# Kernel optimization log

Hardware: AMD Instinct MI355X
Metric: run time of the kernel (lower is better)

The kernel has to match this reference:

```python
import jax, jax.numpy as jnp
import numpy as np

N, E = 50000, 800000
IN, HID, HEADS, OUT = 128, 64, 4, 256
HC = HID * HEADS  # 256
NEG_SLOPE = 0.2
LN_EPS = 1e-5


def setup_inputs() -> dict:
    key = jax.random.key(0)
    ks = jax.random.split(key, 20)
    s = 0.02
    inp = {
        "x": jax.random.normal(ks[0], (N, IN), jnp.float32),
        "edge_index": jax.random.randint(ks[1], (2, E), 0, N, jnp.int64),
        "w_in": jax.random.normal(ks[2], (IN, HID), jnp.float32) * s,
        "b_in": jnp.zeros((HID,), jnp.float32),
        "lin0_w": jax.random.normal(ks[3], (HID, HC), jnp.float32) * s,
        "att_src0": jax.random.normal(ks[4], (HEADS, HID), jnp.float32) * s,
        "att_dst0": jax.random.normal(ks[5], (HEADS, HID), jnp.float32) * s,
        "bias0": jnp.zeros((HC,), jnp.float32),
        "ln0_g": jnp.ones((HC,), jnp.float32),
        "ln0_b": jnp.zeros((HC,), jnp.float32),
        "lin1_w": jax.random.normal(ks[6], (HC, HC), jnp.float32) * s,
        "att_src1": jax.random.normal(ks[7], (HEADS, HID), jnp.float32) * s,
        "att_dst1": jax.random.normal(ks[8], (HEADS, HID), jnp.float32) * s,
        "bias1": jnp.zeros((HC,), jnp.float32),
        "ln1_g": jnp.ones((HC,), jnp.float32),
        "ln1_b": jnp.zeros((HC,), jnp.float32),
        "w_out": jax.random.normal(ks[9], (HC, OUT), jnp.float32) * s,
        "b_out": jnp.zeros((OUT,), jnp.float32),
    }
    return inp


def _gat_conv(x, src, dst, lin_w, att_s, att_d, bias):
    # x: [N, F_in]; src/dst: [E'] (self loops included); output [N, HEADS*HID]
    n = x.shape[0]
    h = (x @ lin_w).reshape(n, HEADS, HID)                     # [N,H,C]
    a_s = jnp.einsum('nhc,hc->nh', h, att_s)                   # [N,H]
    a_d = jnp.einsum('nhc,hc->nh', h, att_d)
    e = jax.nn.leaky_relu(a_s[src] + a_d[dst], NEG_SLOPE)      # [E',H]
    # scatter-softmax over edges grouped by destination node
    m = jax.ops.segment_max(e, dst, num_segments=n)            # [N,H]
    ex = jnp.exp(e - m[dst])
    z = jax.ops.segment_sum(ex, dst, num_segments=n)
    alpha = ex / (z[dst] + 1e-16)                              # [E',H]
    msg = h[src] * alpha[:, :, None]                           # [E',H,C]
    out = jax.ops.segment_sum(msg, dst, num_segments=n)        # [N,H,C]
    return out.reshape(n, HEADS * HID) + bias


def _layernorm(x, g, b):
    mu = x.mean(-1, keepdims=True)
    var = ((x - mu) ** 2).mean(-1, keepdims=True)
    return (x - mu) * jax.lax.rsqrt(var + LN_EPS) * g + b


def reference(x, edge_index, w_in, b_in,
              lin0_w, att_src0, att_dst0, bias0, ln0_g, ln0_b,
              lin1_w, att_src1, att_dst1, bias1, ln1_g, ln1_b,
              w_out, b_out):
    n = x.shape[0]
    # PyG GATConv adds self loops by default
    loop = jnp.arange(n, dtype=edge_index.dtype)
    src = jnp.concatenate([edge_index[0], loop])
    dst = jnp.concatenate([edge_index[1], loop])

    h = jax.nn.relu(x @ w_in + b_in)                           # input_proj + relu
    h = _gat_conv(h, src, dst, lin0_w, att_src0, att_dst0, bias0)
    h = jax.nn.relu(_layernorm(h, ln0_g, ln0_b))               # dropout: eval mode (identity)
    h = _gat_conv(h, src, dst, lin1_w, att_src1, att_dst1, bias1)
    h = jax.nn.relu(_layernorm(h, ln1_g, ln1_b))
    g = h.mean(axis=0)                                         # mean pool over nodes
    return g @ w_out + b_out                                   # [OUT]
```

## Files before the change

kernel.cpp:

```cpp
#include <hip/hip_runtime.h>

#define NN 50000
#define EE 800000
#define EP (EE + NN)
#define NH 4
#define HC 256
#define NOUT 256
#define NEG_SLOPE 0.2f
#define LN_EPS 1e-5f
#define NB 49
#define CHUNK 64
#define NPART 64

typedef unsigned short u16;
typedef __attribute__((ext_vector_type(8))) short bf16x8;
typedef __attribute__((ext_vector_type(8))) unsigned short ushort8;
typedef __attribute__((ext_vector_type(4))) float f32x4;
typedef __attribute__((ext_vector_type(2))) float f32x2;

__device__ __forceinline__ u16 f2bf(float f) {
    unsigned int u = __float_as_uint(f);
    u += 0x7fff + ((u >> 16) & 1);
    return (u16)(u >> 16);
}
__device__ __forceinline__ float bf2f(u16 s) {
    return __uint_as_float(((unsigned int)s) << 16);
}
__device__ __forceinline__ int permL(int s) {
    return (s >> 6) * 64 + (s & 3) * 16 + ((s & 63) >> 2);
}

__global__ void k_prep(const float* __restrict__ w_in, const float* __restrict__ lin0_w,
                       const float* __restrict__ lin1_w,
                       const float* __restrict__ atts0, const float* __restrict__ attd0,
                       const float* __restrict__ bias1, const float* __restrict__ ln1g,
                       const float* __restrict__ ln1b,
                       u16* __restrict__ winT, u16* __restrict__ w0T, u16* __restrict__ w1T,
                       float* __restrict__ avs, float* __restrict__ avd,
                       float* __restrict__ biasP, float* __restrict__ gP, float* __restrict__ bP,
                       int* __restrict__ deg, float* __restrict__ gaccP,
                       const int* __restrict__ raw, int* __restrict__ flag) {
    int b = blockIdx.x, t = threadIdx.x;
    if (b < 352) {
        int i = b * 256 + t;
        if (i < 8192)       { int k = i >> 6,  j = i & 63;  winT[j * 128 + k] = f2bf(w_in[i]); }
        else if (i < 24576) { int i2 = i - 8192;  int k = i2 >> 8, j = i2 & 255; w0T[j * 64 + k]  = f2bf(lin0_w[i2]); }
        else if (i < 90112) { int i2 = i - 24576; int k = i2 >> 8, j = i2 & 255; w1T[j * 256 + k] = f2bf(lin1_w[i2]); }
    } else if (b < 548) {
        int i = (b - 352) * 256 + t;
        if (i < NN) deg[i] = 0;
    } else if (b < 612) {
        gaccP[(b - 548) * 256 + t] = 0.f;
    } else if (b == 612) {
        __shared__ int any;
        if (t == 0) any = 0;
        __syncthreads();
        int found = 0;
        for (int i = t; i < 4096; i += 256)
            if (raw[2 * i + 1] != 0) found = 1;
        if (found) atomicOr(&any, 1);
        __syncthreads();
        if (t == 0) *flag = any;
    } else if (b == 613) {
        int k = t >> 2, h = t & 3;
        float ss = 0.f, dd = 0.f;
        for (int c = 0; c < 64; ++c) {
            float w = lin0_w[k * HC + h * 64 + c];
            ss += w * atts0[h * 64 + c];
            dd += w * attd0[h * 64 + c];
        }
        avs[t] = ss; avd[t] = dd;
    } else {
        int L = permL(t);
        biasP[t] = bias1[L];
        gP[t]    = ln1g[L];
        bP[t]    = ln1b[L];
    }
}

__global__ void k_hist(const int* __restrict__ raw, const int* __restrict__ flag,
                       int* __restrict__ deg) {
    int e = blockIdx.x * blockDim.x + threadIdx.x;
    if (e >= EE) return;
    int d = (*flag) ? raw[EE + e] : raw[2 * (EE + e)];
    atomicAdd(&deg[d], 1);
}

__global__ void k_scanA(const int* __restrict__ deg, int* __restrict__ tmp,
                        int* __restrict__ bsum) {
    __shared__ int ws[16];
    int lane = threadIdx.x & 63, wid = threadIdx.x >> 6;
    int i = blockIdx.x * 1024 + threadIdx.x;
    int x = (i < NN) ? deg[i] + 1 : 0;
    #pragma unroll
    for (int o = 1; o < 64; o <<= 1) {
        int t = __shfl_up(x, o, 64);
        if (lane >= o) x += t;
    }
    if (lane == 63) ws[wid] = x;
    __syncthreads();
    if (wid == 0 && lane < 16) {
        int s = ws[lane];
        #pragma unroll
        for (int o = 1; o < 16; o <<= 1) {
            int t = __shfl_up(s, o, 64);
            if (lane >= o) s += t;
        }
        ws[lane] = s;
    }
    __syncthreads();
    x += (wid > 0) ? ws[wid - 1] : 0;
    if (i < NN) tmp[i] = x;
    if (threadIdx.x == 1023) bsum[blockIdx.x] = x;
}

__global__ void k_scanC(const int* __restrict__ tmp, const int* __restrict__ bsum,
                        const int* __restrict__ deg, int* __restrict__ rowptr,
                        int* __restrict__ cursor) {
    __shared__ int soff;
    if (threadIdx.x == 0) {
        int o = 0;
        for (int j = 0; j < blockIdx.x; ++j) o += bsum[j];
        soff = o;
    }
    __syncthreads();
    int i = blockIdx.x * 1024 + threadIdx.x;
    if (i >= NN) return;
    int fin = tmp[i] + soff;
    rowptr[i + 1] = fin;
    cursor[i] = fin - (deg[i] + 1);
    if (i == 0) rowptr[0] = 0;
}

__global__ void k_scatter(const int* __restrict__ raw, const int* __restrict__ flag,
                          int* __restrict__ cursor, int* __restrict__ esrc) {
    int e = blockIdx.x * blockDim.x + threadIdx.x;
    if (e >= EP) return;
    int s, d;
    if (e >= EE) { s = e - EE; d = s; }
    else if (*flag) { s = raw[e];     d = raw[EE + e]; }
    else            { s = raw[2 * e]; d = raw[2 * (EE + e)]; }
    int pos = atomicAdd(&cursor[d], 1);
    esrc[pos] = s;
}

__global__ void k_proj_mfma(const float* __restrict__ x, const u16* __restrict__ wT,
                            const float* __restrict__ bias,
                            const float* __restrict__ avs, const float* __restrict__ avd,
                            u16* __restrict__ h0,
                            float* __restrict__ as_, float* __restrict__ ad_) {
    __shared__ float4 s_avs[64], s_avd[64];
    int wave = threadIdx.x >> 6, lane = threadIdx.x & 63;
    int lr = lane & 15, lk = lane >> 4;
    if (threadIdx.x < 64) {
        s_avs[threadIdx.x] = *(const float4*)&avs[threadIdx.x * 4];
        s_avd[threadIdx.x] = *(const float4*)&avd[threadIdx.x * 4];
    }
    __syncthreads();
    int rowbase = (blockIdx.x * 4 + wave) * 64;
    f32x4 acc[4][4];
    #pragma unroll
    for (int mf = 0; mf < 4; ++mf)
        #pragma unroll
        for (int nf = 0; nf < 4; ++nf) acc[mf][nf] = (f32x4)0.f;
    for (int kk = 0; kk < 128; kk += 32) {
        bf16x8 a[4], b[4];
        #pragma unroll
        for (int mf = 0; mf < 4; ++mf) {
            int row = rowbase + mf * 16 + lr;
            if (row < NN) {
                float4 v0 = *(const float4*)&x[(size_t)row * 128 + kk + lk * 8];
                float4 v1 = *(const float4*)&x[(size_t)row * 128 + kk + lk * 8 + 4];
                a[mf][0] = (short)f2bf(v0.x); a[mf][1] = (short)f2bf(v0.y);
                a[mf][2] = (short)f2bf(v0.z); a[mf][3] = (short)f2bf(v0.w);
                a[mf][4] = (short)f2bf(v1.x); a[mf][5] = (short)f2bf(v1.y);
                a[mf][6] = (short)f2bf(v1.z); a[mf][7] = (short)f2bf(v1.w);
            } else a[mf] = (bf16x8)(short)0;
        }
        #pragma unroll
        for (int nf = 0; nf < 4; ++nf)
            b[nf] = *(const bf16x8*)&wT[(size_t)(nf * 16 + lr) * 128 + kk + lk * 8];
        #pragma unroll
        for (int mf = 0; mf < 4; ++mf)
            #pragma unroll
            for (int nf = 0; nf < 4; ++nf)
                acc[mf][nf] = __builtin_amdgcn_mfma_f32_16x16x32_bf16(a[mf], b[nf], acc[mf][nf], 0, 0, 0);
    }
    #pragma unroll
    for (int mf = 0; mf < 4; ++mf)
        #pragma unroll
        for (int r = 0; r < 4; ++r) {
            int row = rowbase + mf * 16 + lk * 4 + r;
            float4 ps = make_float4(0.f, 0.f, 0.f, 0.f);
            float4 pd = make_float4(0.f, 0.f, 0.f, 0.f);
            #pragma unroll
            for (int nf = 0; nf < 4; ++nf) {
                int col = nf * 16 + lr;
                float v = fmaxf(acc[mf][nf][r] + bias[col], 0.f);
                if (row < NN) h0[(size_t)row * 64 + col] = f2bf(v);
                float4 vs = s_avs[col], vd = s_avd[col];
                ps.x += v * vs.x; ps.y += v * vs.y; ps.z += v * vs.z; ps.w += v * vs.w;
                pd.x += v * vd.x; pd.y += v * vd.y; pd.z += v * vd.z; pd.w += v * vd.w;
            }
            #pragma unroll
            for (int o = 1; o < 16; o <<= 1) {
                ps.x += __shfl_xor(ps.x, o, 64); ps.y += __shfl_xor(ps.y, o, 64);
                ps.z += __shfl_xor(ps.z, o, 64); ps.w += __shfl_xor(ps.w, o, 64);
                pd.x += __shfl_xor(pd.x, o, 64); pd.y += __shfl_xor(pd.y, o, 64);
                pd.z += __shfl_xor(pd.z, o, 64); pd.w += __shfl_xor(pd.w, o, 64);
            }
            if (lr == 0 && row < NN) {
                *(float4*)&as_[row * NH] = ps;
                *(float4*)&ad_[row * NH] = pd;
            }
        }
}

__global__ void k_agg64(const int* __restrict__ rowptr, const int* __restrict__ esrc,
                        const u16* __restrict__ h0, const float* __restrict__ as_,
                        const float* __restrict__ ad_, u16* __restrict__ agg) {
    __shared__ float sw[4][CHUNK][4];
    __shared__ int   ss[4][CHUNK];
    int wave = threadIdx.x >> 6, lane = threadIdx.x & 63;
    int n = blockIdx.x * 4 + wave;
    int start = rowptr[n], end = rowptr[n + 1];
    float4 adv = *(const float4*)&ad_[n * NH];
    int p = lane & 15, grp = lane >> 4;
    f32x2 acc2[4][2];
    #pragma unroll
    for (int h = 0; h < 4; ++h) {
        acc2[h][0] = (f32x2)0.f;
        acc2[h][1] = (f32x2)0.f;
    }
    float z0 = 0.f, z1 = 0.f, z2 = 0.f, z3 = 0.f;

    for (int base = start; base < end; base += CHUNK) {
        int m = end - base; if (m > CHUNK) m = CHUNK;
        {
            int s = 0; float4 w4 = make_float4(0.f, 0.f, 0.f, 0.f);
            if (lane < m) {
                s = esrc[base + lane];
                float4 asv = *(const float4*)&as_[s * NH];
                float e0 = asv.x + adv.x; e0 = e0 > 0.f ? e0 : e0 * NEG_SLOPE; w4.x = __expf(e0);
                float e1 = asv.y + adv.y; e1 = e1 > 0.f ? e1 : e1 * NEG_SLOPE; w4.y = __expf(e1);
                float e2 = asv.z + adv.z; e2 = e2 > 0.f ? e2 : e2 * NEG_SLOPE; w4.z = __expf(e2);
                float e3 = asv.w + adv.w; e3 = e3 > 0.f ? e3 : e3 * NEG_SLOPE; w4.w = __expf(e3);
            }
            ss[wave][lane] = s;
            *(float4*)&sw[wave][lane][0] = w4;
            z0 += w4.x; z1 += w4.y; z2 += w4.z; z3 += w4.w;
        }
        int e = grp;
        int s = ss[wave][e];
        float4 w4 = *(const float4*)&sw[wave][e][0];
        uint2 hv = *(const uint2*)&h0[(size_t)s * 64 + p * 4];
        int nIter = (m + 3) >> 2;
        for (int it = 0; it < nIter; ++it) {
            int en = (e + 4) & (CHUNK - 1);
            int sn = ss[wave][en];
            float4 w4n = *(const float4*)&sw[wave][en][0];
            uint2 hvn = *(const uint2*)&h0[(size_t)sn * 64 + p * 4];
            f32x2 p01, p23;
            p01[0] = __uint_as_float(hv.x << 16);
            p01[1] = __uint_as_float(hv.x & 0xffff0000u);
            p23[0] = __uint_as_float(hv.y << 16);
            p23[1] = __uint_as_float(hv.y & 0xffff0000u);
            acc2[0][0] += (f32x2)w4.x * p01; acc2[0][1] += (f32x2)w4.x * p23;
            acc2[1][0] += (f32x2)w4.y * p01; acc2[1][1] += (f32x2)w4.y * p23;
            acc2[2][0] += (f32x2)w4.z * p01; acc2[2][1] += (f32x2)w4.z * p23;
            acc2[3][0] += (f32x2)w4.w * p01; acc2[3][1] += (f32x2)w4.w * p23;
            e = en; w4 = w4n; hv = hvn;
        }
    }
    #pragma unroll
    for (int h = 0; h < 4; ++h)
        #pragma unroll
        for (int j = 0; j < 2; ++j) {
            acc2[h][j][0] += __shfl_xor(acc2[h][j][0], 16, 64);
            acc2[h][j][0] += __shfl_xor(acc2[h][j][0], 32, 64);
            acc2[h][j][1] += __shfl_xor(acc2[h][j][1], 16, 64);
            acc2[h][j][1] += __shfl_xor(acc2[h][j][1], 32, 64);
        }
    #pragma unroll
    for (int o = 32; o >= 1; o >>= 1) {
        z0 += __shfl_xor(z0, o, 64);
        z1 += __shfl_xor(z1, o, 64);
        z2 += __shfl_xor(z2, o, 64);
        z3 += __shfl_xor(z3, o, 64);
    }
    if (grp == 0) {
        float iz[4] = {1.f / (z0 + 1e-16f), 1.f / (z1 + 1e-16f),
                       1.f / (z2 + 1e-16f), 1.f / (z3 + 1e-16f)};
        #pragma unroll
        for (int h = 0; h < 4; ++h) {
            ushort4 yv;
            yv.x = f2bf(acc2[h][0][0] * iz[h]);
            yv.y = f2bf(acc2[h][0][1] * iz[h]);
            yv.z = f2bf(acc2[h][1][0] * iz[h]);
            yv.w = f2bf(acc2[h][1][1] * iz[h]);
            *(ushort4*)&agg[(size_t)n * HC + h * 64 + p * 4] = yv;
        }
    }
}

__global__ __launch_bounds__(256) void k_mid(
        const u16* __restrict__ agg, const u16* __restrict__ w0T,
        const float* __restrict__ bias0, const float* __restrict__ g0, const float* __restrict__ b0,
        const u16* __restrict__ w1T,
        const float* __restrict__ atts1, const float* __restrict__ attd1,
        unsigned int* __restrict__ hp8,
        float* __restrict__ as_, float* __restrict__ ad_) {
    __shared__ __align__(16) u16 h1sh[64 * 256];
    __shared__ float stat[64][4][2];
    __shared__ float murs[64][2];
    int wave = threadIdx.x >> 6, lane = threadIdx.x & 63;
    int lr = lane & 15, lk = lane >> 4;
    int rowbase = blockIdx.x * 64;

    f32x4 acc[4][4];
    #pragma unroll
    for (int mf = 0; mf < 4; ++mf)
        #pragma unroll
        for (int nf = 0; nf < 4; ++nf) acc[mf][nf] = (f32x4)0.f;
    for (int kk = 0; kk < 64; kk += 32) {
        bf16x8 a[4], bv[4];
        #pragma unroll
        for (int mf = 0; mf < 4; ++mf) {
            int row = rowbase + mf * 16 + lr;
            a[mf] = (row < NN) ? *(const bf16x8*)&agg[(size_t)row * HC + wave * 64 + kk + lk * 8]
                               : (bf16x8)(short)0;
        }
        #pragma unroll
        for (int nf = 0; nf < 4; ++nf)
            bv[nf] = *(const bf16x8*)&w0T[(size_t)(wave * 64 + nf * 16 + lr) * 64 + kk + lk * 8];
        #pragma unroll
        for (int mf = 0; mf < 4; ++mf)
            #pragma unroll
            for (int nf = 0; nf < 4; ++nf)
                acc[mf][nf] = __builtin_amdgcn_mfma_f32_16x16x32_bf16(a[mf], bv[nf], acc[mf][nf], 0, 0, 0);
    }
    float bcol[4];
    #pragma unroll
    for (int nf = 0; nf < 4; ++nf) bcol[nf] = bias0[wave * 64 + nf * 16 + lr];
    #pragma unroll
    for (int mf = 0; mf < 4; ++mf)
        #pragma unroll
        for (int r = 0; r < 4; ++r) {
            float s = 0.f, q = 0.f;
            #pragma unroll
            for (int nf = 0; nf < 4; ++nf) {
                float xv = acc[mf][nf][r] + bcol[nf];
                s += xv; q += xv * xv;
            }
            #pragma unroll
            for (int o = 1; o < 16; o <<= 1) {
                s += __shfl_xor(s, o, 64);
                q += __shfl_xor(q, o, 64);
            }
            if (lr == 0) {
                int row = mf * 16 + lk * 4 + r;
                stat[row][wave][0] = s;
                stat[row][wave][1] = q;
            }
        }
    __syncthreads();
    if (threadIdx.x < 64) {
        int row = threadIdx.x;
        float S = stat[row][0][0] + stat[row][1][0] + stat[row][2][0] + stat[row][3][0];
        float Q = stat[row][0][1] + stat[row][1][1] + stat[row][2][1] + stat[row][3][1];
        float mu = S * (1.f / HC);
        float var = Q * (1.f / HC) - mu * mu;
        murs[row][0] = mu;
        murs[row][1] = rsqrtf(var + LN_EPS);
    }
    __syncthreads();
    #pragma unroll
    for (int mf = 0; mf < 4; ++mf)
        #pragma unroll
        for (int r = 0; r < 4; ++r) {
            int lrow = mf * 16 + lk * 4 + r;
            float mu = murs[lrow][0], rs = murs[lrow][1];
            #pragma unroll
            for (int nf = 0; nf < 4; ++nf) {
                int col = wave * 64 + nf * 16 + lr;
                float xv = acc[mf][nf][r] + bcol[nf];
                u16 y = f2bf(fmaxf((xv - mu) * rs * g0[col] + b0[col], 0.f));
                int byte = (lrow * 512 + col * 2) ^ ((lrow & 7) << 4);
                *(u16*)((char*)h1sh + byte) = y;
            }
        }
    __syncthreads();

    f32x4 acc2[4][4];
    #pragma unroll
    for (int mf = 0; mf < 4; ++mf)
        #pragma unroll
        for (int nf = 0; nf < 4; ++nf) acc2[mf][nf] = (f32x4)0.f;
    for (int kk = 0; kk < 256; kk += 32) {
        bf16x8 a[4], bv[4];
        #pragma unroll
        for (int mf = 0; mf < 4; ++mf) {
            int row = mf * 16 + lr;
            int byte = (row * 512 + (kk + lk * 8) * 2) ^ ((row & 7) << 4);
            a[mf] = *(const bf16x8*)((const char*)h1sh + byte);
        }
        #pragma unroll
        for (int nf = 0; nf < 4; ++nf)
            bv[nf] = *(const bf16x8*)&w1T[(size_t)(wave * 64 + nf * 16 + lr) * 256 + kk + lk * 8];
        #pragma unroll
        for (int mf = 0; mf < 4; ++mf)
            #pragma unroll
            for (int nf = 0; nf < 4; ++nf)
                acc2[mf][nf] = __builtin_amdgcn_mfma_f32_16x16x32_bf16(a[mf], bv[nf], acc2[mf][nf], 0, 0, 0);
    }
    float asv[4], adv[4];
    #pragma unroll
    for (int nf = 0; nf < 4; ++nf) {
        int col = wave * 64 + nf * 16 + lr;
        asv[nf] = atts1[col];
        adv[nf] = attd1[col];
    }
    #pragma unroll
    for (int mf = 0; mf < 4; ++mf)
        #pragma unroll
        for (int r = 0; r < 4; ++r) {
            int row = rowbase + mf * 16 + lk * 4 + r;
            float v0 = acc2[mf][0][r], v1 = acc2[mf][1][r];
            float v2 = acc2[mf][2][r], v3 = acc2[mf][3][r];
            float ps = v0 * asv[0] + v1 * asv[1] + v2 * asv[2] + v3 * asv[3];
            float pd = v0 * adv[0] + v1 * adv[1] + v2 * adv[2] + v3 * adv[3];
            unsigned int pk = (unsigned int)__builtin_amdgcn_cvt_pk_fp8_f32(v0, v1, 0, false);
            pk = (unsigned int)__builtin_amdgcn_cvt_pk_fp8_f32(v2, v3, (int)pk, true);
            if (row < NN) hp8[(size_t)row * 64 + wave * 16 + lr] = pk;
            #pragma unroll
            for (int o = 1; o < 16; o <<= 1) {
                ps += __shfl_xor(ps, o, 64);
                pd += __shfl_xor(pd, o, 64);
            }
            if (lr == 0 && row < NN) {
                as_[row * NH + wave] = ps;
                ad_[row * NH + wave] = pd;
            }
        }
}

__global__ void k_agg_ln8(const int* __restrict__ rowptr, const int* __restrict__ esrc,
                          const unsigned int* __restrict__ hp8, const float* __restrict__ as_,
                          const float* __restrict__ ad_,
                          const float* __restrict__ biasP, const float* __restrict__ gP,
                          const float* __restrict__ bP, float* __restrict__ gaccP) {
    __shared__ float sw[4][CHUNK][4];
    __shared__ int   ss[4][CHUNK];
    __shared__ float pool[4][16][17];
    int wave = threadIdx.x >> 6, lane = threadIdx.x & 63;
    int n = blockIdx.x * 4 + wave;
    int start = rowptr[n], end = rowptr[n + 1];
    float4 adv = *(const float4*)&ad_[n * NH];
    int p = lane & 15, grp = lane >> 4;
    int c = p * 16, hd = p >> 2;
    f32x2 acc2[8];
    #pragma unroll
    for (int j = 0; j < 8; ++j) acc2[j] = (f32x2)0.f;
    float z0 = 0.f, z1 = 0.f, z2 = 0.f, z3 = 0.f;

    for (int base = start; base < end; base += CHUNK) {
        int m = end - base; if (m > CHUNK) m = CHUNK;
        if (lane < m) {
            int s = esrc[base + lane];
            float4 asv = *(const float4*)&as_[s * NH];
            float e0 = asv.x + adv.x; e0 = e0 > 0.f ? e0 : e0 * NEG_SLOPE; float w0 = __expf(e0);
            float e1 = asv.y + adv.y; e1 = e1 > 0.f ? e1 : e1 * NEG_SLOPE; float w1 = __expf(e1);
            float e2 = asv.z + adv.z; e2 = e2 > 0.f ? e2 : e2 * NEG_SLOPE; float w2 = __expf(e2);
            float e3 = asv.w + adv.w; e3 = e3 > 0.f ? e3 : e3 * NEG_SLOPE; float w3 = __expf(e3);
            ss[wave][lane] = s;
            *(float4*)&sw[wave][lane][0] = make_float4(w0, w1, w2, w3);
            z0 += w0; z1 += w1; z2 += w2; z3 += w3;
        }
        int e = grp;
        bool v = e < m;
        int s = v ? ss[wave][e] : 0;
        float w = v ? sw[wave][e][hd] : 0.f;
        uint4 q = *(const uint4*)&hp8[(size_t)s * 64 + p * 4];
        int nIter = (m + 3) >> 2;
        for (int it = 0; it < nIter; ++it) {
            int en = e + 4;
            bool vn = en < m;
            int sn = vn ? ss[wave][en] : 0;
            float wn = vn ? sw[wave][en][hd] : 0.f;
            uint4 qn = *(const uint4*)&hp8[(size_t)sn * 64 + p * 4];
            f32x2 wv = (f32x2)w;
            acc2[0] += wv * __builtin_amdgcn_cvt_pk_f32_fp8((int)q.x, false);
            acc2[1] += wv * __builtin_amdgcn_cvt_pk_f32_fp8((int)q.x, true);
            acc2[2] += wv * __builtin_amdgcn_cvt_pk_f32_fp8((int)q.y, false);
            acc2[3] += wv * __builtin_amdgcn_cvt_pk_f32_fp8((int)q.y, true);
            acc2[4] += wv * __builtin_amdgcn_cvt_pk_f32_fp8((int)q.z, false);
            acc2[5] += wv * __builtin_amdgcn_cvt_pk_f32_fp8((int)q.z, true);
            acc2[6] += wv * __builtin_amdgcn_cvt_pk_f32_fp8((int)q.w, false);
            acc2[7] += wv * __builtin_amdgcn_cvt_pk_f32_fp8((int)q.w, true);
            e = en; w = wn; q = qn;
        }
    }
    #pragma unroll
    for (int j = 0; j < 8; ++j) {
        acc2[j][0] += __shfl_xor(acc2[j][0], 16, 64);
        acc2[j][0] += __shfl_xor(acc2[j][0], 32, 64);
        acc2[j][1] += __shfl_xor(acc2[j][1], 16, 64);
        acc2[j][1] += __shfl_xor(acc2[j][1], 32, 64);
    }
    #pragma unroll
    for (int o = 32; o >= 1; o >>= 1) {
        z0 += __shfl_xor(z0, o, 64);
        z1 += __shfl_xor(z1, o, 64);
        z2 += __shfl_xor(z2, o, 64);
        z3 += __shfl_xor(z3, o, 64);
    }
    float zh = hd == 0 ? z0 : hd == 1 ? z1 : hd == 2 ? z2 : z3;
    float iz = 1.f / (zh + 1e-16f);
    float xv[16], sum = 0.f;
    #pragma unroll
    for (int k = 0; k < 16; ++k) { xv[k] = acc2[k >> 1][k & 1] * iz + biasP[c + k]; sum += xv[k]; }
    #pragma unroll
    for (int o = 8; o >= 1; o >>= 1) sum += __shfl_xor(sum, o, 64);
    float mu = sum * (1.f / HC);
    float vs = 0.f;
    #pragma unroll
    for (int k = 0; k < 16; ++k) { float d = xv[k] - mu; vs += d * d; }
    #pragma unroll
    for (int o = 8; o >= 1; o >>= 1) vs += __shfl_xor(vs, o, 64);
    float rs = rsqrtf(vs * (1.f / HC) + LN_EPS);
    if (grp == 0) {
        #pragma unroll
        for (int k = 0; k < 16; ++k)
            pool[wave][p][k] = fmaxf((xv[k] - mu) * rs * gP[c + k] + bP[c + k], 0.f);
    }
    __syncthreads();
    int t = threadIdx.x;
    float s = pool[0][t >> 4][t & 15] + pool[1][t >> 4][t & 15]
            + pool[2][t >> 4][t & 15] + pool[3][t >> 4][t & 15];
    atomicAdd(&gaccP[(blockIdx.x & (NPART - 1)) * 256 + t], s);
}

__global__ void k_final(const float* __restrict__ gaccP, const float* __restrict__ w,
                        const float* __restrict__ b, float* __restrict__ out) {
    __shared__ float gs[256];
    int t = threadIdx.x;
    float s = 0.f;
    for (int pp = 0; pp < NPART; ++pp) s += gaccP[pp * 256 + t];
    gs[t] = s;
    __syncthreads();
    float acc = b[t];
    for (int k = 0; k < HC; ++k)
        acc += (gs[k] * (1.f / NN)) * w[permL(k) * NOUT + t];
    out[t] = acc;
}

extern "C" void kernel_launch(void* const* d_in, const int* in_sizes, int n_in,
                              void* d_out, int out_size, void* d_ws, size_t ws_size,
                              hipStream_t stream) {
    const float* x      = (const float*)d_in[0];
    const int*   eiraw  = (const int*)d_in[1];
    const float* w_in   = (const float*)d_in[2];
    const float* b_in   = (const float*)d_in[3];
    const float* lin0_w = (const float*)d_in[4];
    const float* atts0  = (const float*)d_in[5];
    const float* attd0  = (const float*)d_in[6];
    const float* bias0  = (const float*)d_in[7];
    const float* ln0g   = (const float*)d_in[8];
    const float* ln0b   = (const float*)d_in[9];
    const float* lin1_w = (const float*)d_in[10];
    const float* atts1  = (const float*)d_in[11];
    const float* attd1  = (const float*)d_in[12];
    const float* bias1  = (const float*)d_in[13];
    const float* ln1g   = (const float*)d_in[14];
    const float* ln1b   = (const float*)d_in[15];
    const float* w_out  = (const float*)d_in[16];
    const float* b_out  = (const float*)d_in[17];
    float* out = (float*)d_out;

    char* ws = (char*)d_ws;
    size_t off = 0;
    auto alloc = [&](size_t bytes) {
        void* p = ws + off;
        off = (off + bytes + 255) & ~(size_t)255;
        return p;
    };
    int*   esrc   = (int*)  alloc((size_t)EP * 4 + 256);
    int*   deg    = (int*)  alloc((size_t)NN * 4);
    int*   cursor = (int*)  alloc((size_t)NN * 4);
    int*   tmp    = (int*)  alloc((size_t)NN * 4);
    int*   bsum   = (int*)  alloc(64 * 4);
    int*   rowptr = (int*)  alloc((size_t)(NN + 1) * 4);
    int*   flag   = (int*)  alloc(256);
    u16*   winT   = (u16*)  alloc((size_t)64 * 128 * 2);
    u16*   w0T    = (u16*)  alloc((size_t)256 * 64 * 2);
    u16*   w1T    = (u16*)  alloc((size_t)256 * 256 * 2);
    float* avs    = (float*)alloc(64 * 4 * 4);
    float* avd    = (float*)alloc(64 * 4 * 4);
    float* biasP  = (float*)alloc(HC * 4);
    float* gP     = (float*)alloc(HC * 4);
    float* bP     = (float*)alloc(HC * 4);
    u16*   h0b    = (u16*)  alloc((size_t)NN * 64 * 2);
    u16*   hpb    = (u16*)  alloc((size_t)NN * HC * 2);
    unsigned int* hp8 = (unsigned int*)alloc((size_t)NN * 64 * 4);
    float* as_    = (float*)alloc((size_t)NN * NH * 4);
    float* ad_    = (float*)alloc((size_t)NN * NH * 4);
    float* gaccP  = (float*)alloc((size_t)NPART * HC * 4);

    k_prep<<<615, 256, 0, stream>>>(w_in, lin0_w, lin1_w, atts0, attd0, bias1, ln1g, ln1b,
                                    winT, w0T, w1T, avs, avd, biasP, gP, bP,
                                    deg, gaccP, eiraw, flag);
    k_hist<<<(EE + 255) / 256, 256, 0, stream>>>(eiraw, flag, deg);
    k_scanA<<<NB, 1024, 0, stream>>>(deg, tmp, bsum);
    k_scanC<<<NB, 1024, 0, stream>>>(tmp, bsum, deg, rowptr, cursor);
    k_scatter<<<(EP + 255) / 256, 256, 0, stream>>>(eiraw, flag, cursor, esrc);

    k_proj_mfma<<<(NN + 255) / 256, 256, 0, stream>>>(x, winT, b_in, avs, avd, h0b, as_, ad_);

    k_agg64<<<NN / 4, 256, 0, stream>>>(rowptr, esrc, h0b, as_, ad_, hpb);

    k_mid<<<(NN + 63) / 64, 256, 0, stream>>>(hpb, w0T, bias0, ln0g, ln0b,
                                              w1T, atts1, attd1, hp8, as_, ad_);

    k_agg_ln8<<<NN / 4, 256, 0, stream>>>(rowptr, esrc, hp8, as_, ad_, biasP, gP, bP, gaccP);

    k_final<<<1, 256, 0, stream>>>(gaccP, w_out, b_out, out);
}
```

Measured before the change: 282.9 us.

## Fuse layer-0 edge aggregation into mid GEMM kernel via LDS tile; deepen fp8 prefetch

The first-layer attention aggregation now runs inside the mid kernel. Each wave aggregates 16 nodes and writes the normalized bf16 rows into a swizzled shared-memory tile, which the following MFMA matmul reads directly. This removes the global write and re-read of the 50000x256 bf16 intermediate and one kernel launch. In exchange the gather phase runs on far fewer waves (782 blocks instead of 12500), which may weaken latency hiding. Separate attention-score buffers are added because the fused kernel still reads the layer-0 scores while writing the layer-1 ones. The layer-1 aggregation loop also gets a two-deep software prefetch of gathered fp8 rows.

```diff
diff --git a/kernel.cpp b/kernel.cpp
--- a/kernel.cpp
+++ b/kernel.cpp
@@ -216,106 +216,115 @@
         }
 }
 
-__global__ void k_agg64(const int* __restrict__ rowptr, const int* __restrict__ esrc,
-                        const u16* __restrict__ h0, const float* __restrict__ as_,
-                        const float* __restrict__ ad_, u16* __restrict__ agg) {
-    __shared__ float sw[4][CHUNK][4];
-    __shared__ int   ss[4][CHUNK];
-    int wave = threadIdx.x >> 6, lane = threadIdx.x & 63;
-    int n = blockIdx.x * 4 + wave;
-    int start = rowptr[n], end = rowptr[n + 1];
-    float4 adv = *(const float4*)&ad_[n * NH];
-    int p = lane & 15, grp = lane >> 4;
-    f32x2 acc2[4][2];
-    #pragma unroll
-    for (int h = 0; h < 4; ++h) {
-        acc2[h][0] = (f32x2)0.f;
-        acc2[h][1] = (f32x2)0.f;
-    }
-    float z0 = 0.f, z1 = 0.f, z2 = 0.f, z3 = 0.f;
-
-    for (int base = start; base < end; base += CHUNK) {
-        int m = end - base; if (m > CHUNK) m = CHUNK;
-        {
-            int s = 0; float4 w4 = make_float4(0.f, 0.f, 0.f, 0.f);
-            if (lane < m) {
-                s = esrc[base + lane];
-                float4 asv = *(const float4*)&as_[s * NH];
-                float e0 = asv.x + adv.x; e0 = e0 > 0.f ? e0 : e0 * NEG_SLOPE; w4.x = __expf(e0);
-                float e1 = asv.y + adv.y; e1 = e1 > 0.f ? e1 : e1 * NEG_SLOPE; w4.y = __expf(e1);
-                float e2 = asv.z + adv.z; e2 = e2 > 0.f ? e2 : e2 * NEG_SLOPE; w4.z = __expf(e2);
-                float e3 = asv.w + adv.w; e3 = e3 > 0.f ? e3 : e3 * NEG_SLOPE; w4.w = __expf(e3);
-            }
-            ss[wave][lane] = s;
-            *(float4*)&sw[wave][lane][0] = w4;
-            z0 += w4.x; z1 += w4.y; z2 += w4.z; z3 += w4.w;
-        }
-        int e = grp;
-        int s = ss[wave][e];
-        float4 w4 = *(const float4*)&sw[wave][e][0];
-        uint2 hv = *(const uint2*)&h0[(size_t)s * 64 + p * 4];
-        int nIter = (m + 3) >> 2;
-        for (int it = 0; it < nIter; ++it) {
-            int en = (e + 4) & (CHUNK - 1);
-            int sn = ss[wave][en];
-            float4 w4n = *(const float4*)&sw[wave][en][0];
-            uint2 hvn = *(const uint2*)&h0[(size_t)sn * 64 + p * 4];
-            f32x2 p01, p23;
-            p01[0] = __uint_as_float(hv.x << 16);
-            p01[1] = __uint_as_float(hv.x & 0xffff0000u);
-            p23[0] = __uint_as_float(hv.y << 16);
-            p23[1] = __uint_as_float(hv.y & 0xffff0000u);
-            acc2[0][0] += (f32x2)w4.x * p01; acc2[0][1] += (f32x2)w4.x * p23;
-            acc2[1][0] += (f32x2)w4.y * p01; acc2[1][1] += (f32x2)w4.y * p23;
-            acc2[2][0] += (f32x2)w4.z * p01; acc2[2][1] += (f32x2)w4.z * p23;
-            acc2[3][0] += (f32x2)w4.w * p01; acc2[3][1] += (f32x2)w4.w * p23;
-            e = en; w4 = w4n; hv = hvn;
-        }
-    }
-    #pragma unroll
-    for (int h = 0; h < 4; ++h)
-        #pragma unroll
-        for (int j = 0; j < 2; ++j) {
-            acc2[h][j][0] += __shfl_xor(acc2[h][j][0], 16, 64);
-            acc2[h][j][0] += __shfl_xor(acc2[h][j][0], 32, 64);
-            acc2[h][j][1] += __shfl_xor(acc2[h][j][1], 16, 64);
-            acc2[h][j][1] += __shfl_xor(acc2[h][j][1], 32, 64);
-        }
-    #pragma unroll
-    for (int o = 32; o >= 1; o >>= 1) {
-        z0 += __shfl_xor(z0, o, 64);
-        z1 += __shfl_xor(z1, o, 64);
-        z2 += __shfl_xor(z2, o, 64);
-        z3 += __shfl_xor(z3, o, 64);
-    }
-    if (grp == 0) {
-        float iz[4] = {1.f / (z0 + 1e-16f), 1.f / (z1 + 1e-16f),
-                       1.f / (z2 + 1e-16f), 1.f / (z3 + 1e-16f)};
-        #pragma unroll
-        for (int h = 0; h < 4; ++h) {
-            ushort4 yv;
-            yv.x = f2bf(acc2[h][0][0] * iz[h]);
-            yv.y = f2bf(acc2[h][0][1] * iz[h]);
-            yv.z = f2bf(acc2[h][1][0] * iz[h]);
-            yv.w = f2bf(acc2[h][1][1] * iz[h]);
-            *(ushort4*)&agg[(size_t)n * HC + h * 64 + p * 4] = yv;
-        }
-    }
-}
-
-__global__ __launch_bounds__(256) void k_mid(
-        const u16* __restrict__ agg, const u16* __restrict__ w0T,
+__global__ __launch_bounds__(256) void k_agg_mid(
+        const int* __restrict__ rowptr, const int* __restrict__ esrc,
+        const u16* __restrict__ h0, const float* __restrict__ as_,
+        const float* __restrict__ ad_,
+        const u16* __restrict__ w0T,
         const float* __restrict__ bias0, const float* __restrict__ g0, const float* __restrict__ b0,
         const u16* __restrict__ w1T,
         const float* __restrict__ atts1, const float* __restrict__ attd1,
         unsigned int* __restrict__ hp8,
-        float* __restrict__ as_, float* __restrict__ ad_) {
-    __shared__ __align__(16) u16 h1sh[64 * 256];
+        float* __restrict__ as1_, float* __restrict__ ad1_) {
+    __shared__ __align__(16) u16 tile[64 * 256];
+    __shared__ float sw[4][CHUNK][4];
+    __shared__ int   ssx[4][CHUNK];
     __shared__ float stat[64][4][2];
     __shared__ float murs[64][2];
     int wave = threadIdx.x >> 6, lane = threadIdx.x & 63;
     int lr = lane & 15, lk = lane >> 4;
-    int rowbase = blockIdx.x * 64;
+    int p = lane & 15, grp = lane >> 4;
+    int nodebase = blockIdx.x * 64;
+
+    for (int q = 0; q < 16; ++q) {
+        int lrow = wave * 16 + q;
+        int n = nodebase + lrow;
+        if (n >= NN) {
+            if (grp == 0) {
+                #pragma unroll
+                for (int h = 0; h < 4; ++h) {
+                    int byte = (lrow * 512 + (h * 64 + p * 4) * 2) ^ ((lrow & 7) << 4);
+                    *(ushort4*)((char*)tile + byte) = make_ushort4(0, 0, 0, 0);
+                }
+            }
+            continue;
+        }
+        int start = rowptr[n], end = rowptr[n + 1];
+        float4 adv = *(const float4*)&ad_[n * NH];
+        f32x2 acc2[4][2];
+        #pragma unroll
+        for (int h = 0; h < 4; ++h) { acc2[h][0] = (f32x2)0.f; acc2[h][1] = (f32x2)0.f; }
+        float z0 = 0.f, z1 = 0.f, z2 = 0.f, z3 = 0.f;
+        for (int base = start; base < end; base += CHUNK) {
+            int m = end - base; if (m > CHUNK) m = CHUNK;
+            {
+                int s = 0; float4 w4 = make_float4(0.f, 0.f, 0.f, 0.f);
+                if (lane < m) {
+                    s = esrc[base + lane];
+                    float4 asv = *(const float4*)&as_[s * NH];
+                    float e0 = asv.x + adv.x; e0 = e0 > 0.f ? e0 : e0 * NEG_SLOPE; w4.x = __expf(e0);
+                    float e1 = asv.y + adv.y; e1 = e1 > 0.f ? e1 : e1 * NEG_SLOPE; w4.y = __expf(e1);
+                    float e2 = asv.z + adv.z; e2 = e2 > 0.f ? e2 : e2 * NEG_SLOPE; w4.z = __expf(e2);
+                    float e3 = asv.w + adv.w; e3 = e3 > 0.f ? e3 : e3 * NEG_SLOPE; w4.w = __expf(e3);
+                }
+                ssx[wave][lane] = s;
+                *(float4*)&sw[wave][lane][0] = w4;
+                z0 += w4.x; z1 += w4.y; z2 += w4.z; z3 += w4.w;
+            }
+            int e = grp;
+            int s = ssx[wave][e];
+            float4 w4 = *(const float4*)&sw[wave][e][0];
+            uint2 hv = *(const uint2*)&h0[(size_t)s * 64 + p * 4];
+            int nIter = (m + 3) >> 2;
+            for (int it = 0; it < nIter; ++it) {
+                int en = (e + 4) & (CHUNK - 1);
+                int sn = ssx[wave][en];
+                float4 w4n = *(const float4*)&sw[wave][en][0];
+                uint2 hvn = *(const uint2*)&h0[(size_t)sn * 64 + p * 4];
+                f32x2 p01, p23;
+                p01[0] = __uint_as_float(hv.x << 16);
+                p01[1] = __uint_as_float(hv.x & 0xffff0000u);
+                p23[0] = __uint_as_float(hv.y << 16);
+                p23[1] = __uint_as_float(hv.y & 0xffff0000u);
+                acc2[0][0] += (f32x2)w4.x * p01; acc2[0][1] += (f32x2)w4.x * p23;
+                acc2[1][0] += (f32x2)w4.y * p01; acc2[1][1] += (f32x2)w4.y * p23;
+                acc2[2][0] += (f32x2)w4.z * p01; acc2[2][1] += (f32x2)w4.z * p23;
+                acc2[3][0] += (f32x2)w4.w * p01; acc2[3][1] += (f32x2)w4.w * p23;
+                e = en; w4 = w4n; hv = hvn;
+            }
+        }
+        #pragma unroll
+        for (int h = 0; h < 4; ++h)
+            #pragma unroll
+            for (int j = 0; j < 2; ++j) {
+                acc2[h][j][0] += __shfl_xor(acc2[h][j][0], 16, 64);
+                acc2[h][j][0] += __shfl_xor(acc2[h][j][0], 32, 64);
+                acc2[h][j][1] += __shfl_xor(acc2[h][j][1], 16, 64);
+                acc2[h][j][1] += __shfl_xor(acc2[h][j][1], 32, 64);
+            }
+        #pragma unroll
+        for (int o = 32; o >= 1; o >>= 1) {
+            z0 += __shfl_xor(z0, o, 64);
+            z1 += __shfl_xor(z1, o, 64);
+            z2 += __shfl_xor(z2, o, 64);
+            z3 += __shfl_xor(z3, o, 64);
+        }
+        if (grp == 0) {
+            float iz[4] = {1.f / (z0 + 1e-16f), 1.f / (z1 + 1e-16f),
+                           1.f / (z2 + 1e-16f), 1.f / (z3 + 1e-16f)};
+            #pragma unroll
+            for (int h = 0; h < 4; ++h) {
+                ushort4 yv;
+                yv.x = f2bf(acc2[h][0][0] * iz[h]);
+                yv.y = f2bf(acc2[h][0][1] * iz[h]);
+                yv.z = f2bf(acc2[h][1][0] * iz[h]);
+                yv.w = f2bf(acc2[h][1][1] * iz[h]);
+                int byte = (lrow * 512 + (h * 64 + p * 4) * 2) ^ ((lrow & 7) << 4);
+                *(ushort4*)((char*)tile + byte) = yv;
+            }
+        }
+    }
+    __syncthreads();
 
     f32x4 acc[4][4];
     #pragma unroll
@@ -326,9 +335,9 @@
         bf16x8 a[4], bv[4];
         #pragma unroll
         for (int mf = 0; mf < 4; ++mf) {
-            int row = rowbase + mf * 16 + lr;
-            a[mf] = (row < NN) ? *(const bf16x8*)&agg[(size_t)row * HC + wave * 64 + kk + lk * 8]
-                               : (bf16x8)(short)0;
+            int lrow = mf * 16 + lr;
+            int byte = (lrow * 512 + (wave * 64 + kk + lk * 8) * 2) ^ ((lrow & 7) << 4);
+            a[mf] = *(const bf16x8*)((const char*)tile + byte);
         }
         #pragma unroll
         for (int nf = 0; nf < 4; ++nf)
@@ -386,7 +395,7 @@
                 float xv = acc[mf][nf][r] + bcol[nf];
                 u16 y = f2bf(fmaxf((xv - mu) * rs * g0[col] + b0[col], 0.f));
                 int byte = (lrow * 512 + col * 2) ^ ((lrow & 7) << 4);
-                *(u16*)((char*)h1sh + byte) = y;
+                *(u16*)((char*)tile + byte) = y;
             }
         }
     __syncthreads();
@@ -400,9 +409,9 @@
         bf16x8 a[4], bv[4];
         #pragma unroll
         for (int mf = 0; mf < 4; ++mf) {
-            int row = mf * 16 + lr;
-            int byte = (row * 512 + (kk + lk * 8) * 2) ^ ((row & 7) << 4);
-            a[mf] = *(const bf16x8*)((const char*)h1sh + byte);
+            int lrow = mf * 16 + lr;
+            int byte = (lrow * 512 + (kk + lk * 8) * 2) ^ ((lrow & 7) << 4);
+            a[mf] = *(const bf16x8*)((const char*)tile + byte);
         }
         #pragma unroll
         for (int nf = 0; nf < 4; ++nf)
@@ -424,7 +433,7 @@
     for (int mf = 0; mf < 4; ++mf)
         #pragma unroll
         for (int r = 0; r < 4; ++r) {
-            int row = rowbase + mf * 16 + lk * 4 + r;
+            int row = nodebase + mf * 16 + lk * 4 + r;
             float v0 = acc2[mf][0][r], v1 = acc2[mf][1][r];
             float v2 = acc2[mf][2][r], v3 = acc2[mf][3][r];
             float ps = v0 * asv[0] + v1 * asv[1] + v2 * asv[2] + v3 * asv[3];
@@ -438,8 +447,8 @@
                 pd += __shfl_xor(pd, o, 64);
             }
             if (lr == 0 && row < NN) {
-                as_[row * NH + wave] = ps;
-                ad_[row * NH + wave] = pd;
+                as1_[row * NH + wave] = ps;
+                ad1_[row * NH + wave] = pd;
             }
         }
 }
@@ -477,27 +486,34 @@
             z0 += w0; z1 += w1; z2 += w2; z3 += w3;
         }
         int e = grp;
-        bool v = e < m;
-        int s = v ? ss[wave][e] : 0;
-        float w = v ? sw[wave][e][hd] : 0.f;
-        uint4 q = *(const uint4*)&hp8[(size_t)s * 64 + p * 4];
+        bool vA = e < m;
+        int sA = vA ? ss[wave][e] : 0;
+        float wA = vA ? sw[wave][e][hd] : 0.f;
+        uint4 qA = *(const uint4*)&hp8[(size_t)sA * 64 + p * 4];
+        int eB = e + 4;
+        bool vB = eB < m;
+        int sB = vB ? ss[wave][eB] : 0;
+        float wB = vB ? sw[wave][eB][hd] : 0.f;
+        uint4 qB = *(const uint4*)&hp8[(size_t)sB * 64 + p * 4];
         int nIter = (m + 3) >> 2;
         for (int it = 0; it < nIter; ++it) {
-            int en = e + 4;
+            int en = e + 8;
             bool vn = en < m;
             int sn = vn ? ss[wave][en] : 0;
             float wn = vn ? sw[wave][en][hd] : 0.f;
             uint4 qn = *(const uint4*)&hp8[(size_t)sn * 64 + p * 4];
-            f32x2 wv = (f32x2)w;
-            acc2[0] += wv * __builtin_amdgcn_cvt_pk_f32_fp8((int)q.x, false);
-            acc2[1] += wv * __builtin_amdgcn_cvt_pk_f32_fp8((int)q.x, true);
-            acc2[2] += wv * __builtin_amdgcn_cvt_pk_f32_fp8((int)q.y, false);
-            acc2[3] += wv * __builtin_amdgcn_cvt_pk_f32_fp8((int)q.y, true);
-            acc2[4] += wv * __builtin_amdgcn_cvt_pk_f32_fp8((int)q.z, false);
-            acc2[5] += wv * __builtin_amdgcn_cvt_pk_f32_fp8((int)q.z, true);
-            acc2[6] += wv * __builtin_amdgcn_cvt_pk_f32_fp8((int)q.w, false);
-            acc2[7] += wv * __builtin_amdgcn_cvt_pk_f32_fp8((int)q.w, true);
-            e = en; w = wn; q = qn;
+            f32x2 wv = (f32x2)wA;
+            acc2[0] += wv * __builtin_amdgcn_cvt_pk_f32_fp8((int)qA.x, false);
+            acc2[1] += wv * __builtin_amdgcn_cvt_pk_f32_fp8((int)qA.x, true);
+            acc2[2] += wv * __builtin_amdgcn_cvt_pk_f32_fp8((int)qA.y, false);
+            acc2[3] += wv * __builtin_amdgcn_cvt_pk_f32_fp8((int)qA.y, true);
+            acc2[4] += wv * __builtin_amdgcn_cvt_pk_f32_fp8((int)qA.z, false);
+            acc2[5] += wv * __builtin_amdgcn_cvt_pk_f32_fp8((int)qA.z, true);
+            acc2[6] += wv * __builtin_amdgcn_cvt_pk_f32_fp8((int)qA.w, false);
+            acc2[7] += wv * __builtin_amdgcn_cvt_pk_f32_fp8((int)qA.w, true);
+            e += 4;
+            qA = qB; wA = wB;
+            qB = qn; wB = wn;
         }
     }
     #pragma unroll
@@ -600,10 +616,11 @@
     float* gP     = (float*)alloc(HC * 4);
     float* bP     = (float*)alloc(HC * 4);
     u16*   h0b    = (u16*)  alloc((size_t)NN * 64 * 2);
-    u16*   hpb    = (u16*)  alloc((size_t)NN * HC * 2);
     unsigned int* hp8 = (unsigned int*)alloc((size_t)NN * 64 * 4);
     float* as_    = (float*)alloc((size_t)NN * NH * 4);
     float* ad_    = (float*)alloc((size_t)NN * NH * 4);
+    float* as1_   = (float*)alloc((size_t)NN * NH * 4);
+    float* ad1_   = (float*)alloc((size_t)NN * NH * 4);
     float* gaccP  = (float*)alloc((size_t)NPART * HC * 4);
 
     k_prep<<<615, 256, 0, stream>>>(w_in, lin0_w, lin1_w, atts0, attd0, bias1, ln1g, ln1b,
@@ -616,12 +633,11 @@
 
     k_proj_mfma<<<(NN + 255) / 256, 256, 0, stream>>>(x, winT, b_in, avs, avd, h0b, as_, ad_);
 
-    k_agg64<<<NN / 4, 256, 0, stream>>>(rowptr, esrc, h0b, as_, ad_, hpb);
-
-    k_mid<<<(NN + 63) / 64, 256, 0, stream>>>(hpb, w0T, bias0, ln0g, ln0b,
-                                              w1T, atts1, attd1, hp8, as_, ad_);
-
-    k_agg_ln8<<<NN / 4, 256, 0, stream>>>(rowptr, esrc, hp8, as_, ad_, biasP, gP, bP, gaccP);
+    k_agg_mid<<<(NN + 63) / 64, 256, 0, stream>>>(rowptr, esrc, h0b, as_, ad_,
+                                                  w0T, bias0, ln0g, ln0b,
+                                                  w1T, atts1, attd1, hp8, as1_, ad1_);
+
+    k_agg_ln8<<<NN / 4, 256, 0, stream>>>(rowptr, esrc, hp8, as1_, ad1_, biasP, gP, bP, gaccP);
 
     k_final<<<1, 256, 0, stream>>>(gaccP, w_out, b_out, out);
 }
```

New measurement: 345.9 us. 22.2% more time.

## Store layer-0 features as fp8 and deepen gather prefetch in layer-1 aggregation

Applied to the files above, without the earlier changes.

The input projection now packs its 64 ReLU outputs per node into fp8 (four values per 32-bit word) instead of bf16, halving the bytes gathered per edge in the first aggregation. Because the packed order interleaves columns, the lin0 weight transpose is permuted to match. The second aggregation kernel now keeps two gathers in flight instead of one to hide memory latency. Separate attention-score buffers are used for layer 1. Using fp8 for the hidden features lowers precision and may move the output toward the tolerance limit.

```diff
diff --git a/kernel.cpp b/kernel.cpp
--- a/kernel.cpp
+++ b/kernel.cpp
@@ -44,7 +44,11 @@
     if (b < 352) {
         int i = b * 256 + t;
         if (i < 8192)       { int k = i >> 6,  j = i & 63;  winT[j * 128 + k] = f2bf(w_in[i]); }
-        else if (i < 24576) { int i2 = i - 8192;  int k = i2 >> 8, j = i2 & 255; w0T[j * 64 + k]  = f2bf(lin0_w[i2]); }
+        else if (i < 24576) {
+            int i2 = i - 8192;  int k = i2 >> 8, j = i2 & 255;
+            int s = ((k & 15) << 2) | (k >> 4);
+            w0T[j * 64 + s] = f2bf(lin0_w[i2]);
+        }
         else if (i < 90112) { int i2 = i - 24576; int k = i2 >> 8, j = i2 & 255; w1T[j * 256 + k] = f2bf(lin1_w[i2]); }
     } else if (b < 548) {
         int i = (b - 352) * 256 + t;
@@ -147,7 +151,7 @@
 __global__ void k_proj_mfma(const float* __restrict__ x, const u16* __restrict__ wT,
                             const float* __restrict__ bias,
                             const float* __restrict__ avs, const float* __restrict__ avd,
-                            u16* __restrict__ h0,
+                            unsigned int* __restrict__ h08,
                             float* __restrict__ as_, float* __restrict__ ad_) {
     __shared__ float4 s_avs[64], s_avd[64];
     int wave = threadIdx.x >> 6, lane = threadIdx.x & 63;
@@ -193,15 +197,19 @@
             int row = rowbase + mf * 16 + lk * 4 + r;
             float4 ps = make_float4(0.f, 0.f, 0.f, 0.f);
             float4 pd = make_float4(0.f, 0.f, 0.f, 0.f);
+            float vv[4];
             #pragma unroll
             for (int nf = 0; nf < 4; ++nf) {
                 int col = nf * 16 + lr;
                 float v = fmaxf(acc[mf][nf][r] + bias[col], 0.f);
-                if (row < NN) h0[(size_t)row * 64 + col] = f2bf(v);
+                vv[nf] = v;
                 float4 vs = s_avs[col], vd = s_avd[col];
                 ps.x += v * vs.x; ps.y += v * vs.y; ps.z += v * vs.z; ps.w += v * vs.w;
                 pd.x += v * vd.x; pd.y += v * vd.y; pd.z += v * vd.z; pd.w += v * vd.w;
             }
+            unsigned int pk = (unsigned int)__builtin_amdgcn_cvt_pk_fp8_f32(vv[0], vv[1], 0, false);
+            pk = (unsigned int)__builtin_amdgcn_cvt_pk_fp8_f32(vv[2], vv[3], (int)pk, true);
+            if (row < NN) h08[(size_t)row * 16 + lr] = pk;
             #pragma unroll
             for (int o = 1; o < 16; o <<= 1) {
                 ps.x += __shfl_xor(ps.x, o, 64); ps.y += __shfl_xor(ps.y, o, 64);
@@ -217,7 +225,7 @@
 }
 
 __global__ void k_agg64(const int* __restrict__ rowptr, const int* __restrict__ esrc,
-                        const u16* __restrict__ h0, const float* __restrict__ as_,
+                        const unsigned int* __restrict__ h08, const float* __restrict__ as_,
                         const float* __restrict__ ad_, u16* __restrict__ agg) {
     __shared__ float sw[4][CHUNK][4];
     __shared__ int   ss[4][CHUNK];
@@ -228,10 +236,7 @@
     int p = lane & 15, grp = lane >> 4;
     f32x2 acc2[4][2];
     #pragma unroll
-    for (int h = 0; h < 4; ++h) {
-        acc2[h][0] = (f32x2)0.f;
-        acc2[h][1] = (f32x2)0.f;
-    }
+    for (int h = 0; h < 4; ++h) { acc2[h][0] = (f32x2)0.f; acc2[h][1] = (f32x2)0.f; }
     float z0 = 0.f, z1 = 0.f, z2 = 0.f, z3 = 0.f;
 
     for (int base = start; base < end; base += CHUNK) {
@@ -253,23 +258,20 @@
         int e = grp;
         int s = ss[wave][e];
         float4 w4 = *(const float4*)&sw[wave][e][0];
-        uint2 hv = *(const uint2*)&h0[(size_t)s * 64 + p * 4];
+        unsigned int q = h08[s * 16 + p];
         int nIter = (m + 3) >> 2;
         for (int it = 0; it < nIter; ++it) {
             int en = (e + 4) & (CHUNK - 1);
             int sn = ss[wave][en];
             float4 w4n = *(const float4*)&sw[wave][en][0];
-            uint2 hvn = *(const uint2*)&h0[(size_t)sn * 64 + p * 4];
-            f32x2 p01, p23;
-            p01[0] = __uint_as_float(hv.x << 16);
-            p01[1] = __uint_as_float(hv.x & 0xffff0000u);
-            p23[0] = __uint_as_float(hv.y << 16);
-            p23[1] = __uint_as_float(hv.y & 0xffff0000u);
+            unsigned int qn = h08[sn * 16 + p];
+            f32x2 p01 = __builtin_amdgcn_cvt_pk_f32_fp8((int)q, false);
+            f32x2 p23 = __builtin_amdgcn_cvt_pk_f32_fp8((int)q, true);
             acc2[0][0] += (f32x2)w4.x * p01; acc2[0][1] += (f32x2)w4.x * p23;
             acc2[1][0] += (f32x2)w4.y * p01; acc2[1][1] += (f32x2)w4.y * p23;
             acc2[2][0] += (f32x2)w4.z * p01; acc2[2][1] += (f32x2)w4.z * p23;
             acc2[3][0] += (f32x2)w4.w * p01; acc2[3][1] += (f32x2)w4.w * p23;
-            e = en; w4 = w4n; hv = hvn;
+            e = en; w4 = w4n; q = qn;
         }
     }
     #pragma unroll
@@ -477,27 +479,34 @@
             z0 += w0; z1 += w1; z2 += w2; z3 += w3;
         }
         int e = grp;
-        bool v = e < m;
-        int s = v ? ss[wave][e] : 0;
-        float w = v ? sw[wave][e][hd] : 0.f;
-        uint4 q = *(const uint4*)&hp8[(size_t)s * 64 + p * 4];
+        bool vA = e < m;
+        int sA = vA ? ss[wave][e] : 0;
+        float wA = vA ? sw[wave][e][hd] : 0.f;
+        uint4 qA = *(const uint4*)&hp8[(size_t)sA * 64 + p * 4];
+        int eB = e + 4;
+        bool vB = eB < m;
+        int sB = vB ? ss[wave][eB] : 0;
+        float wB = vB ? sw[wave][eB][hd] : 0.f;
+        uint4 qB = *(const uint4*)&hp8[(size_t)sB * 64 + p * 4];
         int nIter = (m + 3) >> 2;
         for (int it = 0; it < nIter; ++it) {
-            int en = e + 4;
+            int en = e + 8;
             bool vn = en < m;
             int sn = vn ? ss[wave][en] : 0;
             float wn = vn ? sw[wave][en][hd] : 0.f;
             uint4 qn = *(const uint4*)&hp8[(size_t)sn * 64 + p * 4];
-            f32x2 wv = (f32x2)w;
-            acc2[0] += wv * __builtin_amdgcn_cvt_pk_f32_fp8((int)q.x, false);
-            acc2[1] += wv * __builtin_amdgcn_cvt_pk_f32_fp8((int)q.x, true);
-            acc2[2] += wv * __builtin_amdgcn_cvt_pk_f32_fp8((int)q.y, false);
-            acc2[3] += wv * __builtin_amdgcn_cvt_pk_f32_fp8((int)q.y, true);
-            acc2[4] += wv * __builtin_amdgcn_cvt_pk_f32_fp8((int)q.z, false);
-            acc2[5] += wv * __builtin_amdgcn_cvt_pk_f32_fp8((int)q.z, true);
-            acc2[6] += wv * __builtin_amdgcn_cvt_pk_f32_fp8((int)q.w, false);
-            acc2[7] += wv * __builtin_amdgcn_cvt_pk_f32_fp8((int)q.w, true);
-            e = en; w = wn; q = qn;
+            f32x2 wv = (f32x2)wA;
+            acc2[0] += wv * __builtin_amdgcn_cvt_pk_f32_fp8((int)qA.x, false);
+            acc2[1] += wv * __builtin_amdgcn_cvt_pk_f32_fp8((int)qA.x, true);
+            acc2[2] += wv * __builtin_amdgcn_cvt_pk_f32_fp8((int)qA.y, false);
+            acc2[3] += wv * __builtin_amdgcn_cvt_pk_f32_fp8((int)qA.y, true);
+            acc2[4] += wv * __builtin_amdgcn_cvt_pk_f32_fp8((int)qA.z, false);
+            acc2[5] += wv * __builtin_amdgcn_cvt_pk_f32_fp8((int)qA.z, true);
+            acc2[6] += wv * __builtin_amdgcn_cvt_pk_f32_fp8((int)qA.w, false);
+            acc2[7] += wv * __builtin_amdgcn_cvt_pk_f32_fp8((int)qA.w, true);
+            e += 4;
+            qA = qB; wA = wB;
+            qB = qn; wB = wn;
         }
     }
     #pragma unroll
@@ -599,11 +608,13 @@
     float* biasP  = (float*)alloc(HC * 4);
     float* gP     = (float*)alloc(HC * 4);
     float* bP     = (float*)alloc(HC * 4);
-    u16*   h0b    = (u16*)  alloc((size_t)NN * 64 * 2);
+    unsigned int* h08 = (unsigned int*)alloc((size_t)NN * 16 * 4);
     u16*   hpb    = (u16*)  alloc((size_t)NN * HC * 2);
     unsigned int* hp8 = (unsigned int*)alloc((size_t)NN * 64 * 4);
     float* as_    = (float*)alloc((size_t)NN * NH * 4);
     float* ad_    = (float*)alloc((size_t)NN * NH * 4);
+    float* as1_   = (float*)alloc((size_t)NN * NH * 4);
+    float* ad1_   = (float*)alloc((size_t)NN * NH * 4);
     float* gaccP  = (float*)alloc((size_t)NPART * HC * 4);
 
     k_prep<<<615, 256, 0, stream>>>(w_in, lin0_w, lin1_w, atts0, attd0, bias1, ln1g, ln1b,
@@ -614,14 +625,14 @@
     k_scanC<<<NB, 1024, 0, stream>>>(tmp, bsum, deg, rowptr, cursor);
     k_scatter<<<(EP + 255) / 256, 256, 0, stream>>>(eiraw, flag, cursor, esrc);
 
-    k_proj_mfma<<<(NN + 255) / 256, 256, 0, stream>>>(x, winT, b_in, avs, avd, h0b, as_, ad_);
-
-    k_agg64<<<NN / 4, 256, 0, stream>>>(rowptr, esrc, h0b, as_, ad_, hpb);
+    k_proj_mfma<<<(NN + 255) / 256, 256, 0, stream>>>(x, winT, b_in, avs, avd, h08, as_, ad_);
+
+    k_agg64<<<NN / 4, 256, 0, stream>>>(rowptr, esrc, h08, as_, ad_, hpb);
 
     k_mid<<<(NN + 63) / 64, 256, 0, stream>>>(hpb, w0T, bias0, ln0g, ln0b,
-                                              w1T, atts1, attd1, hp8, as_, ad_);
-
-    k_agg_ln8<<<NN / 4, 256, 0, stream>>>(rowptr, esrc, hp8, as_, ad_, biasP, gP, bP, gaccP);
+                                              w1T, atts1, attd1, hp8, as1_, ad1_);
+
+    k_agg_ln8<<<NN / 4, 256, 0, stream>>>(rowptr, esrc, hp8, as1_, ad1_, biasP, gP, bP, gaccP);
 
     k_final<<<1, 256, 0, stream>>>(gaccP, w_out, b_out, out);
 }
```

After: 277.9 us. Within noise of the previous version (-1.8%).
